# Optimization experiments

Hardware: AMD Instinct MI355X
Metric: run time of the kernel (lower is better)

Reference implementation:

```python
import jax, jax.numpy as jnp
import numpy as np

DT = 1e-3
MAX_UPDATE = 0.1


def setup_inputs() -> dict:
    key = jax.random.key(0)
    k1, k2 = jax.random.split(key)
    B, T = 512, 8192
    inputs = jax.random.normal(k1, (B, T, 2), dtype=jnp.float32)
    # learned 2x2 kernel, keras 'uniform' init ~ U(-0.05, 0.05)
    A = jax.random.uniform(k2, (2, 2), dtype=jnp.float32, minval=-0.05, maxval=0.05)
    # physical model coefficients (from coeffs tuple)
    C = jnp.eye(2, dtype=jnp.float32)
    D = 1e-3 * jnp.eye(2, dtype=jnp.float32)
    return {"inputs": inputs, "A": A, "C": C, "D": D}


def reference(inputs, A, C, D):
    # inputs: [B, T, 2] measurement increments dy
    B = inputs.shape[0]
    # initial state per GRNNmodel.initial_state: x0=[1,0], cov0=eye(2)
    x0 = jnp.tile(jnp.array([[1.0, 0.0]], dtype=inputs.dtype), (B, 1))      # [B,2]
    cov0 = jnp.tile(jnp.eye(2, dtype=inputs.dtype)[None], (B, 1, 1))        # [B,2,2]

    Ct = C.T
    Dt = D.T

    def step(carry, dy):
        x, cov = carry                                   # [B,2], [B,2,2]
        out = jnp.einsum('ij,bj->bi', C, x) * DT         # output uses pre-update state
        xicov = cov @ Ct + Dt                            # [B,2,2]
        A_minus_xiC = A - xicov @ C                      # [B,2,2]
        dx = jnp.einsum('bij,bj->bi', A_minus_xiC, x) * DT \
             + jnp.einsum('bij,bj->bi', xicov, dy)
        x_new = x + jnp.clip(dx, -MAX_UPDATE, MAX_UPDATE)
        cov_dt = (jnp.einsum('ij,bjk->bik', A, cov)
                  + jnp.einsum('bij,kj->bik', cov, A)    # cov @ A^T
                  + D
                  - xicov @ jnp.swapaxes(xicov, 1, 2))
        cov_new = jnp.clip(cov + cov_dt * DT, -1.0, 1.0)
        return (x_new, cov_new), out

    dys = jnp.swapaxes(inputs, 0, 1)                     # [T,B,2]
    _, outs = jax.lax.scan(step, (x0, cov0), dys)
    return jnp.swapaxes(outs, 0, 1)                      # [B,T,2]
```

## Files before the change

kernel.cpp:

```cpp
#include <hip/hip_runtime.h>


#define DT_C 1e-3f
#define MAXU 0.1f
#define T_LEN 8192
#define T4 (T_LEN / 2)
#define CHUNK 256
#define G_CHUNK (CHUNK / 2)
#define NCHUNK (T_LEN / CHUNK)

__device__ __forceinline__ float clipf(float v, float lo, float hi) {
    return fminf(fmaxf(v, lo), hi);
}
#define MEDU(x) __builtin_amdgcn_fmed3f((x), -MAXU, MAXU)
#define SB() __builtin_amdgcn_sched_barrier(0)

__global__ __launch_bounds__(128, 1) void grnn_fused(
    const float* __restrict__ inp, const float* __restrict__ Am,
    const float* __restrict__ Cm, const float* __restrict__ Dm,
    float* __restrict__ out)
{
    __shared__ float pb0[CHUNK + 1];
    __shared__ float pb1[CHUNK + 1];
    __shared__ float pb2[CHUNK + 1];
    __shared__ float4 pbufg[CHUNK];
    __shared__ float4 wlds[2][CHUNK * 2];
    const int tid = threadIdx.x;

    if (tid < 64) {
        const int lane = tid;
        const float a00 = Am[0], a01 = Am[1], a10 = Am[2], a11 = Am[3];
        const float c00 = Cm[0], c01 = Cm[1], c10 = Cm[2], c11 = Cm[3];
        const float d00 = Dm[0], d01 = Dm[1], d10 = Dm[2], d11 = Dm[3];
        const bool special = (c00 == 1.f) && (c01 == 0.f) && (c10 == 0.f) &&
                             (c11 == 1.f) && (d01 == 0.f) && (d10 == 0.f);
        const float adt00 = a00 * DT_C, adt01 = a01 * DT_C;
        const float adt10 = a10 * DT_C, adt11 = a11 * DT_C;

        if (special) {
            const float K00 = 1.f + 2.f * adt00, A2dt01 = 2.f * adt01;
            const float K11 = 1.f + 2.f * adt11, A2dt10 = 2.f * adt10;
            const float K01 = 1.f + (a00 + a11) * DT_C;
            const float cd0 = DT_C * d00, cd1 = DT_C * d11;
            float p00 = 1.f, p01 = 0.f, p11 = 1.f;

#define PSTEP(I)                                                              \
            {                                                                 \
                const float xi00 = p00 + d00;                                 \
                const float xi11 = p11 + d11;                                 \
                const float s2  = p01 * p01;                                  \
                const float q00 = fmaf(xi00, xi00, s2);                       \
                const float q11 = fmaf(xi11, xi11, s2);                       \
                const float q01 = p01 * (xi00 + xi11);                        \
                const float t00 = fmaf(K00, p00, fmaf(A2dt01, p01, cd0));     \
                const float t11 = fmaf(A2dt10, p01, fmaf(K11, p11, cd1));     \
                const float t01 = fmaf(adt10, p00,                            \
                                       fmaf(K01, p01, adt01 * p11));          \
                p00 = fmaf(-DT_C, q00, t00);                                  \
                p01 = fmaf(-DT_C, q01, t01);                                  \
                p11 = fmaf(-DT_C, q11, t11);                                  \
                pb0[(I) + 1] = p00;                                           \
                pb1[(I) + 1] = p01;                                           \
                pb2[(I) + 1] = p11;                                           \
            }

            for (int it = 0; it <= NCHUNK; ++it) {
                if (it < NCHUNK) {
                    if (lane == 0) {
                        pb0[0] = p00; pb1[0] = p01; pb2[0] = p11;
                        for (int i = 0; i < CHUNK; i += 8) {
                            PSTEP(i)     PSTEP(i + 1) PSTEP(i + 2) PSTEP(i + 3)
                            PSTEP(i + 4) PSTEP(i + 5) PSTEP(i + 6) PSTEP(i + 7)
                        }
                    }
                    __builtin_amdgcn_wave_barrier();
                    float4* dst = wlds[it & 1];
#pragma unroll
                    for (int k = 0; k < 4; ++k) {
                        const int i = k * 64 + lane;
                        const float pv0 = pb0[i], pv1 = pb1[i], pv2 = pb2[i];
                        const float xi00 = pv0 + d00, xi01 = pv1, xi11 = pv2 + d11;
                        float4 mv, xv;
                        mv.x = fmaf(-DT_C, xi00, adt00);
                        mv.y = fmaf(-DT_C, xi01, adt10);
                        mv.z = fmaf(-DT_C, xi01, adt01);
                        mv.w = fmaf(-DT_C, xi11, adt11);
                        xv = make_float4(xi00, xi01, xi01, xi11);
                        dst[2 * i]     = mv;
                        dst[2 * i + 1] = xv;
                    }
                }
                __syncthreads();
            }
#undef PSTEP
        } else {
            float p00 = 1.f, p01 = 0.f, p10 = 0.f, p11 = 1.f;
            for (int it = 0; it <= NCHUNK; ++it) {
                if (it < NCHUNK) {
                    if (lane == 0) {
                        for (int i = 0; i < CHUNK; ++i) {
                            pbufg[i] = make_float4(p00, p01, p10, p11);
                            const float xi00 = p00*c00 + p01*c01 + d00;
                            const float xi01 = p00*c10 + p01*c11 + d10;
                            const float xi10 = p10*c00 + p11*c01 + d01;
                            const float xi11 = p10*c10 + p11*c11 + d11;
                            const float g00 = a00*p00 + a01*p10 + p00*a00 + p01*a01 + d00 - (xi00*xi00 + xi01*xi01);
                            const float g01 = a00*p01 + a01*p11 + p00*a10 + p01*a11 + d01 - (xi00*xi10 + xi01*xi11);
                            const float g10 = a10*p00 + a11*p10 + p10*a00 + p11*a01 + d10 - (xi10*xi00 + xi11*xi01);
                            const float g11 = a10*p01 + a11*p11 + p10*a10 + p11*a11 + d11 - (xi10*xi10 + xi11*xi11);
                            p00 = clipf(p00 + g00 * DT_C, -1.f, 1.f);
                            p01 = clipf(p01 + g01 * DT_C, -1.f, 1.f);
                            p10 = clipf(p10 + g10 * DT_C, -1.f, 1.f);
                            p11 = clipf(p11 + g11 * DT_C, -1.f, 1.f);
                        }
                    }
                    __builtin_amdgcn_wave_barrier();
                    float4* dst = wlds[it & 1];
#pragma unroll
                    for (int k = 0; k < 4; ++k) {
                        const int i = k * 64 + lane;
                        const float4 pv = pbufg[i];
                        const float xi00 = pv.x*c00 + pv.y*c01 + d00;
                        const float xi01 = pv.x*c10 + pv.y*c11 + d10;
                        const float xi10 = pv.z*c00 + pv.w*c01 + d01;
                        const float xi11 = pv.z*c10 + pv.w*c11 + d11;
                        const float m00 = a00 - (xi00*c00 + xi01*c10);
                        const float m01 = a01 - (xi00*c01 + xi01*c11);
                        const float m10 = a10 - (xi10*c00 + xi11*c10);
                        const float m11 = a11 - (xi10*c01 + xi11*c11);
                        float4 mv, xv;
                        mv.x = m00 * DT_C; mv.y = m10 * DT_C;
                        mv.z = m01 * DT_C; mv.w = m11 * DT_C;
                        xv = make_float4(xi00, xi10, xi01, xi11);
                        dst[2 * i]     = mv;
                        dst[2 * i + 1] = xv;
                    }
                }
                __syncthreads();
            }
        }
    } else {
        const int lane = tid - 64;
        const int b = blockIdx.x * 64 + lane;
        const float cdt00 = Cm[0] * DT_C, cdt01 = Cm[1] * DT_C;
        const float cdt10 = Cm[2] * DT_C, cdt11 = Cm[3] * DT_C;
        const float4* __restrict__ in4 =
            reinterpret_cast<const float4*>(inp) + (size_t)b * T4;
        float4* __restrict__ out4 =
            reinterpret_cast<float4*>(out) + (size_t)b * T4;

        float x0 = 1.f, x1 = 0.f;
        float4 d0 = in4[0], d1 = in4[1], d2 = in4[2], d3 = in4[3];
        float4 d4 = in4[4], d5 = in4[5], d6 = in4[6], d7 = in4[7];
        float4 s0a, s0b, s0c, s0d, s1a, s1b, s1c, s1d;
        float4 t0a, t0b, t0c, t0d, t1a, t1b, t1c, t1d;

#define WLG(P, G)                                                             \
        { P##a = wbuf[4*(G)];   P##b = wbuf[4*(G)+1];                         \
          P##c = wbuf[4*(G)+2]; P##d = wbuf[4*(G)+3]; }

#define GRANC(P, DJ, OG)                                                      \
        {                                                                     \
            const float4 dyv = DJ;                                            \
            float4 ov;                                                        \
            ov.x = fmaf(cdt00, x0, cdt01 * x1);                               \
            ov.y = fmaf(cdt10, x0, cdt11 * x1);                               \
            float e0 = fmaf(P##b.x, dyv.x, P##b.z * dyv.y);                   \
            float e1 = fmaf(P##b.y, dyv.x, P##b.w * dyv.y);                   \
            float dx0 = fmaf(P##a.x, x0, fmaf(P##a.z, x1, e0));               \
            float dx1 = fmaf(P##a.y, x0, fmaf(P##a.w, x1, e1));               \
            x0 += MEDU(dx0);                                                  \
            x1 += MEDU(dx1);                                                  \
            ov.z = fmaf(cdt00, x0, cdt01 * x1);                               \
            ov.w = fmaf(cdt10, x0, cdt11 * x1);                               \
            e0 = fmaf(P##d.x, dyv.z, P##d.z * dyv.w);                         \
            e1 = fmaf(P##d.y, dyv.z, P##d.w * dyv.w);                         \
            dx0 = fmaf(P##c.x, x0, fmaf(P##c.z, x1, e0));                     \
            dx1 = fmaf(P##c.y, x0, fmaf(P##c.w, x1, e1));                     \
            x0 += MEDU(dx0);                                                  \
            x1 += MEDU(dx1);                                                  \
            out4[OG] = ov;                                                    \
            const int nog = (OG) + 8;                                         \
            DJ = in4[nog < T4 ? nog : (T4 - 1)];                              \
        }

        for (int it = 0; it <= NCHUNK; ++it) {
            if (it > 0) {
                const int cc = it - 1;
                const float4* wbuf = wlds[cc & 1];
                const int ogc = cc * G_CHUNK;
                WLG(s0, 0) WLG(s1, 1)
                SB();
                for (int q = 0; q < G_CHUNK / 8; ++q) {
                    const int g = 8 * q;
                    const int og = ogc + g;
                    WLG(t0, g + 2) WLG(t1, g + 3)
                    SB();
                    GRANC(s0, d0, og)     GRANC(s1, d1, og + 1)
                    SB();
                    WLG(s0, g + 4) WLG(s1, g + 5)
                    SB();
                    GRANC(t0, d2, og + 2) GRANC(t1, d3, og + 3)
                    SB();
                    WLG(t0, g + 6) WLG(t1, g + 7)
                    SB();
                    GRANC(s0, d4, og + 4) GRANC(s1, d5, og + 5)
                    SB();
                    {
                        const int gn0 = (g + 8 < G_CHUNK) ? (g + 8) : (G_CHUNK - 1);
                        const int gn1 = (g + 9 < G_CHUNK) ? (g + 9) : (G_CHUNK - 1);
                        WLG(s0, gn0) WLG(s1, gn1)
                    }
                    SB();
                    GRANC(t0, d6, og + 6) GRANC(t1, d7, og + 7)
                    SB();
                }
            }
            __syncthreads();
        }
#undef GRANC
#undef WLG
    }
}

__global__ __launch_bounds__(64) void grnn_mono(
    const float* __restrict__ inp, const float* __restrict__ Am,
    const float* __restrict__ Cm, const float* __restrict__ Dm,
    float* __restrict__ out, int B)
{
    const int b = blockIdx.x * blockDim.x + threadIdx.x;
    if (b >= B) return;
    const float a00 = Am[0], a01 = Am[1], a10 = Am[2], a11 = Am[3];
    const float c00 = Cm[0], c01 = Cm[1], c10 = Cm[2], c11 = Cm[3];
    const float d00 = Dm[0], d01 = Dm[1], d10 = Dm[2], d11 = Dm[3];
    float x0 = 1.0f, x1 = 0.0f;
    float p00 = 1.0f, p01 = 0.0f, p10 = 0.0f, p11 = 1.0f;
    const float2* __restrict__ in2 = reinterpret_cast<const float2*>(inp) + (size_t)b * T_LEN;
    float2* __restrict__ out2 = reinterpret_cast<float2*>(out) + (size_t)b * T_LEN;
#pragma unroll 4
    for (int t = 0; t < T_LEN; ++t) {
        float2 o;
        o.x = (c00 * x0 + c01 * x1) * DT_C;
        o.y = (c10 * x0 + c11 * x1) * DT_C;
        out2[t] = o;
        const float xi00 = p00 * c00 + p01 * c01 + d00;
        const float xi01 = p00 * c10 + p01 * c11 + d10;
        const float xi10 = p10 * c00 + p11 * c01 + d01;
        const float xi11 = p10 * c10 + p11 * c11 + d11;
        const float m00 = a00 - (xi00 * c00 + xi01 * c10);
        const float m01 = a01 - (xi00 * c01 + xi01 * c11);
        const float m10 = a10 - (xi10 * c00 + xi11 * c10);
        const float m11 = a11 - (xi10 * c01 + xi11 * c11);
        const float2 dy = in2[t];
        float dx0 = (m00 * x0 + m01 * x1) * DT_C + xi00 * dy.x + xi01 * dy.y;
        float dx1 = (m10 * x0 + m11 * x1) * DT_C + xi10 * dy.x + xi11 * dy.y;
        x0 += clipf(dx0, -MAXU, MAXU);
        x1 += clipf(dx1, -MAXU, MAXU);
        const float g00 = a00*p00 + a01*p10 + p00*a00 + p01*a01 + d00 - (xi00*xi00 + xi01*xi01);
        const float g01 = a00*p01 + a01*p11 + p00*a10 + p01*a11 + d01 - (xi00*xi10 + xi01*xi11);
        const float g10 = a10*p00 + a11*p10 + p10*a00 + p11*a01 + d10 - (xi10*xi00 + xi11*xi01);
        const float g11 = a10*p01 + a11*p11 + p10*a10 + p11*a11 + d11 - (xi10*xi10 + xi11*xi11);
        p00 = clipf(p00 + g00 * DT_C, -1.0f, 1.0f);
        p01 = clipf(p01 + g01 * DT_C, -1.0f, 1.0f);
        p10 = clipf(p10 + g10 * DT_C, -1.0f, 1.0f);
        p11 = clipf(p11 + g11 * DT_C, -1.0f, 1.0f);
    }
}

extern "C" void kernel_launch(void* const* d_in, const int* in_sizes, int n_in,
                              void* d_out, int out_size, void* d_ws, size_t ws_size,
                              hipStream_t stream) {
    const float* inp = (const float*)d_in[0];
    const float* Am  = (const float*)d_in[1];
    const float* Cm  = (const float*)d_in[2];
    const float* Dm  = (const float*)d_in[3];
    float* out = (float*)d_out;
    const int B = in_sizes[0] / (T_LEN * 2);

    if ((B % 64) == 0) {
        hipLaunchKernelGGL(grnn_fused, dim3(B / 64), dim3(128), 0, stream,
                           inp, Am, Cm, Dm, out);
    } else {
        hipLaunchKernelGGL(grnn_mono, dim3((B + 63) / 64), dim3(64), 0, stream,
                           inp, Am, Cm, Dm, out, B);
    }
}
```

Baseline: 537.7 us.

## Batch covariance stores into vector LDS writes and add idle waves

The scalar covariance recurrence in lane 0 now collects eight consecutive states in float4 registers and writes them to LDS with vector stores, replacing three scalar stores per step. The shared buffers drop their +1 offset, so each chunk begins with the state before the step. The block grows to four waves: wave 0 runs the per-batch state update, wave 1 produces the covariance, and waves 2 and 3 only join the barriers, which may change how the waves are placed on SIMDs. The next-input global load in the state update is also issued at the start of each step to give it more time in flight.

```diff
diff --git a/kernel.cpp b/kernel.cpp
--- a/kernel.cpp
+++ b/kernel.cpp
@@ -9,26 +9,29 @@
 #define G_CHUNK (CHUNK / 2)
 #define NCHUNK (T_LEN / CHUNK)
 
+typedef float vfloat4 __attribute__((ext_vector_type(4)));
+
 __device__ __forceinline__ float clipf(float v, float lo, float hi) {
     return fminf(fmaxf(v, lo), hi);
 }
 #define MEDU(x) __builtin_amdgcn_fmed3f((x), -MAXU, MAXU)
 #define SB() __builtin_amdgcn_sched_barrier(0)
 
-__global__ __launch_bounds__(128, 1) void grnn_fused(
+__global__ __launch_bounds__(256, 1) void grnn_fused(
     const float* __restrict__ inp, const float* __restrict__ Am,
     const float* __restrict__ Cm, const float* __restrict__ Dm,
     float* __restrict__ out)
 {
-    __shared__ float pb0[CHUNK + 1];
-    __shared__ float pb1[CHUNK + 1];
-    __shared__ float pb2[CHUNK + 1];
+    __shared__ alignas(16) float pb0[CHUNK];
+    __shared__ alignas(16) float pb1[CHUNK];
+    __shared__ alignas(16) float pb2[CHUNK];
     __shared__ float4 pbufg[CHUNK];
     __shared__ float4 wlds[2][CHUNK * 2];
     const int tid = threadIdx.x;
-
-    if (tid < 64) {
-        const int lane = tid;
+    const int wv = tid >> 6;
+
+    if (wv == 1) {
+        const int lane = tid & 63;
         const float a00 = Am[0], a01 = Am[1], a10 = Am[2], a11 = Am[3];
         const float c00 = Cm[0], c01 = Cm[1], c10 = Cm[2], c11 = Cm[3];
         const float d00 = Dm[0], d01 = Dm[1], d10 = Dm[2], d11 = Dm[3];
@@ -44,8 +47,9 @@
             const float cd0 = DT_C * d00, cd1 = DT_C * d11;
             float p00 = 1.f, p01 = 0.f, p11 = 1.f;
 
-#define PSTEP(I)                                                              \
+#define PSTEP(Q0, Q1, Q2, F)                                                  \
             {                                                                 \
+                Q0.F = p00; Q1.F = p01; Q2.F = p11;                           \
                 const float xi00 = p00 + d00;                                 \
                 const float xi11 = p11 + d11;                                 \
                 const float s2  = p01 * p01;                                  \
@@ -59,18 +63,33 @@
                 p00 = fmaf(-DT_C, q00, t00);                                  \
                 p01 = fmaf(-DT_C, q01, t01);                                  \
                 p11 = fmaf(-DT_C, q11, t11);                                  \
-                pb0[(I) + 1] = p00;                                           \
-                pb1[(I) + 1] = p01;                                           \
-                pb2[(I) + 1] = p11;                                           \
+            }
+
+#define PBLOCK8(QA0, QA1, QA2, QB0, QB1, QB2, I)                              \
+            {                                                                 \
+                PSTEP(QA0, QA1, QA2, x) PSTEP(QA0, QA1, QA2, y)               \
+                PSTEP(QA0, QA1, QA2, z) PSTEP(QA0, QA1, QA2, w)               \
+                PSTEP(QB0, QB1, QB2, x) PSTEP(QB0, QB1, QB2, y)               \
+                PSTEP(QB0, QB1, QB2, z) PSTEP(QB0, QB1, QB2, w)               \
+                *(vfloat4*)&pb0[(I)]     = QA0;                               \
+                *(vfloat4*)&pb0[(I) + 4] = QB0;                               \
+                *(vfloat4*)&pb1[(I)]     = QA1;                               \
+                *(vfloat4*)&pb1[(I) + 4] = QB1;                               \
+                *(vfloat4*)&pb2[(I)]     = QA2;                               \
+                *(vfloat4*)&pb2[(I) + 4] = QB2;                               \
             }
 
             for (int it = 0; it <= NCHUNK; ++it) {
                 if (it < NCHUNK) {
                     if (lane == 0) {
-                        pb0[0] = p00; pb1[0] = p01; pb2[0] = p11;
-                        for (int i = 0; i < CHUNK; i += 8) {
-                            PSTEP(i)     PSTEP(i + 1) PSTEP(i + 2) PSTEP(i + 3)
-                            PSTEP(i + 4) PSTEP(i + 5) PSTEP(i + 6) PSTEP(i + 7)
+                        for (int i = 0; i < CHUNK; i += 16) {
+                            vfloat4 qa0, qa1, qa2, qb0, qb1, qb2;
+                            vfloat4 qc0, qc1, qc2, qd0, qd1, qd2;
+                            PBLOCK8(qa0, qa1, qa2, qb0, qb1, qb2, i)
+                            PBLOCK8(qc0, qc1, qc2, qd0, qd1, qd2, i + 8)
+                            asm volatile("" ::
+                                "v"(qa0), "v"(qa1), "v"(qa2),
+                                "v"(qb0), "v"(qb1), "v"(qb2));
                         }
                     }
                     __builtin_amdgcn_wave_barrier();
@@ -92,6 +111,7 @@
                 }
                 __syncthreads();
             }
+#undef PBLOCK8
 #undef PSTEP
         } else {
             float p00 = 1.f, p01 = 0.f, p10 = 0.f, p11 = 1.f;
@@ -139,8 +159,8 @@
                 __syncthreads();
             }
         }
-    } else {
-        const int lane = tid - 64;
+    } else if (wv == 0) {
+        const int lane = tid;
         const int b = blockIdx.x * 64 + lane;
         const float cdt00 = Cm[0] * DT_C, cdt01 = Cm[1] * DT_C;
         const float cdt10 = Cm[2] * DT_C, cdt11 = Cm[3] * DT_C;
@@ -162,6 +182,8 @@
 #define GRANC(P, DJ, OG)                                                      \
         {                                                                     \
             const float4 dyv = DJ;                                            \
+            const int nog = (OG) + 8;                                         \
+            DJ = in4[nog < T4 ? nog : (T4 - 1)];                              \
             float4 ov;                                                        \
             ov.x = fmaf(cdt00, x0, cdt01 * x1);                               \
             ov.y = fmaf(cdt10, x0, cdt11 * x1);                               \
@@ -180,8 +202,6 @@
             x0 += MEDU(dx0);                                                  \
             x1 += MEDU(dx1);                                                  \
             out4[OG] = ov;                                                    \
-            const int nog = (OG) + 8;                                         \
-            DJ = in4[nog < T4 ? nog : (T4 - 1)];                              \
         }
 
         for (int it = 0; it <= NCHUNK; ++it) {
@@ -220,6 +240,8 @@
         }
 #undef GRANC
 #undef WLG
+    } else {
+        for (int it = 0; it <= NCHUNK; ++it) __syncthreads();
     }
 }
 
@@ -278,7 +300,7 @@
     const int B = in_sizes[0] / (T_LEN * 2);
 
     if ((B % 64) == 0) {
-        hipLaunchKernelGGL(grnn_fused, dim3(B / 64), dim3(128), 0, stream,
+        hipLaunchKernelGGL(grnn_fused, dim3(B / 64), dim3(256), 0, stream,
                            inp, Am, Cm, Dm, out);
     } else {
         hipLaunchKernelGGL(grnn_mono, dim3((B + 63) / 64), dim3(64), 0, stream,
```

After: 497.3 us. -7.5%, faster.

## Split fused kernel into covariance precompute, transposed-layout scan, and transpose kernels

Applied to the files above, without the earlier changes.

The fused producer/consumer kernel is replaced by a pipeline of separate kernels. First the batch-independent covariance recurrence runs serially to produce chunk boundary states, while the input is transposed to time-major layout in the same launch. Next, per-step weight tables are expanded in parallel across chunks into global memory. Then a scan kernel reads the transposed inputs with coalesced loads and writes time-major output, and a final kernel transposes the output back. This removes the per-chunk block barriers and LDS handoff and makes the per-step loads coalesced. The cost is extra launches, two full transposes through global memory, and a serial covariance pass that now runs ahead of the scan instead of overlapping with it.

```diff
diff --git a/kernel.cpp b/kernel.cpp
--- a/kernel.cpp
+++ b/kernel.cpp
@@ -6,29 +6,53 @@
 #define T_LEN 8192
 #define T4 (T_LEN / 2)
 #define CHUNK 256
-#define G_CHUNK (CHUNK / 2)
 #define NCHUNK (T_LEN / CHUNK)
+#define BROWS 512
 
 __device__ __forceinline__ float clipf(float v, float lo, float hi) {
     return fminf(fmaxf(v, lo), hi);
 }
 #define MEDU(x) __builtin_amdgcn_fmed3f((x), -MAXU, MAXU)
-#define SB() __builtin_amdgcn_sched_barrier(0)
-
-__global__ __launch_bounds__(128, 1) void grnn_fused(
-    const float* __restrict__ inp, const float* __restrict__ Am,
-    const float* __restrict__ Cm, const float* __restrict__ Dm,
-    float* __restrict__ out)
-{
-    __shared__ float pb0[CHUNK + 1];
-    __shared__ float pb1[CHUNK + 1];
-    __shared__ float pb2[CHUNK + 1];
-    __shared__ float4 pbufg[CHUNK];
-    __shared__ float4 wlds[2][CHUNK * 2];
-    const int tid = threadIdx.x;
-
-    if (tid < 64) {
-        const int lane = tid;
+
+#define RSTEP_S()                                                             \
+    {                                                                         \
+        const float xi00 = p00 + d00;                                         \
+        const float xi11 = p11 + d11;                                         \
+        const float s2   = p01 * p01;                                         \
+        const float q00  = fmaf(xi00, xi00, s2);                              \
+        const float q11  = fmaf(xi11, xi11, s2);                              \
+        const float q01  = p01 * (xi00 + xi11);                               \
+        const float t00  = fmaf(K00, p00, fmaf(A2dt01, p01, cd0));            \
+        const float t11  = fmaf(A2dt10, p01, fmaf(K11, p11, cd1));            \
+        const float t01  = fmaf(adt10, p00, fmaf(K01, p01, adt01 * p11));     \
+        p00 = fmaf(-DT_C, q00, t00);                                          \
+        p01 = fmaf(-DT_C, q01, t01);                                          \
+        p11 = fmaf(-DT_C, q11, t11);                                          \
+    }
+
+#define RSTEP_G()                                                             \
+    {                                                                         \
+        const float xi00 = p00*c00 + p01*c01 + d00;                           \
+        const float xi01 = p00*c10 + p01*c11 + d10;                           \
+        const float xi10 = p10*c00 + p11*c01 + d01;                           \
+        const float xi11 = p10*c10 + p11*c11 + d11;                           \
+        const float g00 = a00*p00 + a01*p10 + p00*a00 + p01*a01 + d00 - (xi00*xi00 + xi01*xi01); \
+        const float g01 = a00*p01 + a01*p11 + p00*a10 + p01*a11 + d01 - (xi00*xi10 + xi01*xi11); \
+        const float g10 = a10*p00 + a11*p10 + p10*a00 + p11*a01 + d10 - (xi10*xi00 + xi11*xi01); \
+        const float g11 = a10*p01 + a11*p11 + p10*a10 + p11*a11 + d11 - (xi10*xi10 + xi11*xi11); \
+        p00 = clipf(p00 + g00 * DT_C, -1.f, 1.f);                             \
+        p01 = clipf(p01 + g01 * DT_C, -1.f, 1.f);                             \
+        p10 = clipf(p10 + g10 * DT_C, -1.f, 1.f);                             \
+        p11 = clipf(p11 + g11 * DT_C, -1.f, 1.f);                             \
+    }
+
+__global__ __launch_bounds__(256) void transpose_in_a1(
+    const float4* __restrict__ src, float4* __restrict__ dst,
+    const float* __restrict__ Am, const float* __restrict__ Cm,
+    const float* __restrict__ Dm, float4* __restrict__ bnd, int do_tr)
+{
+    if ((int)blockIdx.x == (int)gridDim.x - 1) {
+        if (blockIdx.y != 0 || threadIdx.x != 0) return;
         const float a00 = Am[0], a01 = Am[1], a10 = Am[2], a11 = Am[3];
         const float c00 = Cm[0], c01 = Cm[1], c10 = Cm[2], c11 = Cm[3];
         const float d00 = Dm[0], d01 = Dm[1], d10 = Dm[2], d11 = Dm[3];
@@ -36,191 +60,188 @@
                              (c11 == 1.f) && (d01 == 0.f) && (d10 == 0.f);
         const float adt00 = a00 * DT_C, adt01 = a01 * DT_C;
         const float adt10 = a10 * DT_C, adt11 = a11 * DT_C;
-
+        (void)adt00; (void)adt11;
         if (special) {
             const float K00 = 1.f + 2.f * adt00, A2dt01 = 2.f * adt01;
             const float K11 = 1.f + 2.f * adt11, A2dt10 = 2.f * adt10;
             const float K01 = 1.f + (a00 + a11) * DT_C;
             const float cd0 = DT_C * d00, cd1 = DT_C * d11;
             float p00 = 1.f, p01 = 0.f, p11 = 1.f;
-
-#define PSTEP(I)                                                              \
-            {                                                                 \
-                const float xi00 = p00 + d00;                                 \
-                const float xi11 = p11 + d11;                                 \
-                const float s2  = p01 * p01;                                  \
-                const float q00 = fmaf(xi00, xi00, s2);                       \
-                const float q11 = fmaf(xi11, xi11, s2);                       \
-                const float q01 = p01 * (xi00 + xi11);                        \
-                const float t00 = fmaf(K00, p00, fmaf(A2dt01, p01, cd0));     \
-                const float t11 = fmaf(A2dt10, p01, fmaf(K11, p11, cd1));     \
-                const float t01 = fmaf(adt10, p00,                            \
-                                       fmaf(K01, p01, adt01 * p11));          \
-                p00 = fmaf(-DT_C, q00, t00);                                  \
-                p01 = fmaf(-DT_C, q01, t01);                                  \
-                p11 = fmaf(-DT_C, q11, t11);                                  \
-                pb0[(I) + 1] = p00;                                           \
-                pb1[(I) + 1] = p01;                                           \
-                pb2[(I) + 1] = p11;                                           \
+            for (int c = 0; c < NCHUNK; ++c) {
+                bnd[c] = make_float4(p00, p01, p11, 0.f);
+                for (int i = 0; i < CHUNK; i += 8) {
+                    RSTEP_S() RSTEP_S() RSTEP_S() RSTEP_S()
+                    RSTEP_S() RSTEP_S() RSTEP_S() RSTEP_S()
+                }
             }
-
-            for (int it = 0; it <= NCHUNK; ++it) {
-                if (it < NCHUNK) {
-                    if (lane == 0) {
-                        pb0[0] = p00; pb1[0] = p01; pb2[0] = p11;
-                        for (int i = 0; i < CHUNK; i += 8) {
-                            PSTEP(i)     PSTEP(i + 1) PSTEP(i + 2) PSTEP(i + 3)
-                            PSTEP(i + 4) PSTEP(i + 5) PSTEP(i + 6) PSTEP(i + 7)
-                        }
-                    }
-                    __builtin_amdgcn_wave_barrier();
-                    float4* dst = wlds[it & 1];
-#pragma unroll
-                    for (int k = 0; k < 4; ++k) {
-                        const int i = k * 64 + lane;
-                        const float pv0 = pb0[i], pv1 = pb1[i], pv2 = pb2[i];
-                        const float xi00 = pv0 + d00, xi01 = pv1, xi11 = pv2 + d11;
-                        float4 mv, xv;
-                        mv.x = fmaf(-DT_C, xi00, adt00);
-                        mv.y = fmaf(-DT_C, xi01, adt10);
-                        mv.z = fmaf(-DT_C, xi01, adt01);
-                        mv.w = fmaf(-DT_C, xi11, adt11);
-                        xv = make_float4(xi00, xi01, xi01, xi11);
-                        dst[2 * i]     = mv;
-                        dst[2 * i + 1] = xv;
-                    }
-                }
-                __syncthreads();
-            }
-#undef PSTEP
         } else {
             float p00 = 1.f, p01 = 0.f, p10 = 0.f, p11 = 1.f;
-            for (int it = 0; it <= NCHUNK; ++it) {
-                if (it < NCHUNK) {
-                    if (lane == 0) {
-                        for (int i = 0; i < CHUNK; ++i) {
-                            pbufg[i] = make_float4(p00, p01, p10, p11);
-                            const float xi00 = p00*c00 + p01*c01 + d00;
-                            const float xi01 = p00*c10 + p01*c11 + d10;
-                            const float xi10 = p10*c00 + p11*c01 + d01;
-                            const float xi11 = p10*c10 + p11*c11 + d11;
-                            const float g00 = a00*p00 + a01*p10 + p00*a00 + p01*a01 + d00 - (xi00*xi00 + xi01*xi01);
-                            const float g01 = a00*p01 + a01*p11 + p00*a10 + p01*a11 + d01 - (xi00*xi10 + xi01*xi11);
-                            const float g10 = a10*p00 + a11*p10 + p10*a00 + p11*a01 + d10 - (xi10*xi00 + xi11*xi01);
-                            const float g11 = a10*p01 + a11*p11 + p10*a10 + p11*a11 + d11 - (xi10*xi10 + xi11*xi11);
-                            p00 = clipf(p00 + g00 * DT_C, -1.f, 1.f);
-                            p01 = clipf(p01 + g01 * DT_C, -1.f, 1.f);
-                            p10 = clipf(p10 + g10 * DT_C, -1.f, 1.f);
-                            p11 = clipf(p11 + g11 * DT_C, -1.f, 1.f);
-                        }
-                    }
-                    __builtin_amdgcn_wave_barrier();
-                    float4* dst = wlds[it & 1];
-#pragma unroll
-                    for (int k = 0; k < 4; ++k) {
-                        const int i = k * 64 + lane;
-                        const float4 pv = pbufg[i];
-                        const float xi00 = pv.x*c00 + pv.y*c01 + d00;
-                        const float xi01 = pv.x*c10 + pv.y*c11 + d10;
-                        const float xi10 = pv.z*c00 + pv.w*c01 + d01;
-                        const float xi11 = pv.z*c10 + pv.w*c11 + d11;
-                        const float m00 = a00 - (xi00*c00 + xi01*c10);
-                        const float m01 = a01 - (xi00*c01 + xi01*c11);
-                        const float m10 = a10 - (xi10*c00 + xi11*c10);
-                        const float m11 = a11 - (xi10*c01 + xi11*c11);
-                        float4 mv, xv;
-                        mv.x = m00 * DT_C; mv.y = m10 * DT_C;
-                        mv.z = m01 * DT_C; mv.w = m11 * DT_C;
-                        xv = make_float4(xi00, xi10, xi01, xi11);
-                        dst[2 * i]     = mv;
-                        dst[2 * i + 1] = xv;
-                    }
+            for (int c = 0; c < NCHUNK; ++c) {
+                bnd[c] = make_float4(p00, p01, p10, p11);
+                for (int i = 0; i < CHUNK; i += 4) {
+                    RSTEP_G() RSTEP_G() RSTEP_G() RSTEP_G()
                 }
-                __syncthreads();
             }
         }
+        return;
+    }
+    if (!do_tr) return;
+    __shared__ float4 tile[32][33];
+    const int tx = threadIdx.x & 31;
+    const int ty = threadIdx.x >> 5;
+    const int c0 = blockIdx.x * 32;
+    const int r0 = blockIdx.y * 32;
+#pragma unroll
+    for (int i = 0; i < 32; i += 8)
+        tile[ty + i][tx] = src[(size_t)(r0 + ty + i) * T4 + (c0 + tx)];
+    __syncthreads();
+#pragma unroll
+    for (int i = 0; i < 32; i += 8)
+        dst[(size_t)(c0 + ty + i) * BROWS + (r0 + tx)] = tile[tx][ty + i];
+}
+
+__global__ __launch_bounds__(64) void expand_w(
+    const float* __restrict__ Am, const float* __restrict__ Cm,
+    const float* __restrict__ Dm, const float4* __restrict__ bnd,
+    float4* __restrict__ wst)
+{
+    if (threadIdx.x != 0) return;
+    const int c = blockIdx.x;
+    const float a00 = Am[0], a01 = Am[1], a10 = Am[2], a11 = Am[3];
+    const float c00 = Cm[0], c01 = Cm[1], c10 = Cm[2], c11 = Cm[3];
+    const float d00 = Dm[0], d01 = Dm[1], d10 = Dm[2], d11 = Dm[3];
+    const bool special = (c00 == 1.f) && (c01 == 0.f) && (c10 == 0.f) &&
+                         (c11 == 1.f) && (d01 == 0.f) && (d10 == 0.f);
+    const float adt00 = a00 * DT_C, adt01 = a01 * DT_C;
+    const float adt10 = a10 * DT_C, adt11 = a11 * DT_C;
+    float4* wout = wst + (size_t)c * (CHUNK * 2);
+    const float4 s = bnd[c];
+    if (special) {
+        const float K00 = 1.f + 2.f * adt00, A2dt01 = 2.f * adt01;
+        const float K11 = 1.f + 2.f * adt11, A2dt10 = 2.f * adt10;
+        const float K01 = 1.f + (a00 + a11) * DT_C;
+        const float cd0 = DT_C * d00, cd1 = DT_C * d11;
+        float p00 = s.x, p01 = s.y, p11 = s.z;
+#pragma unroll 4
+        for (int i = 0; i < CHUNK; ++i) {
+            const float xi00 = p00 + d00, xi01 = p01, xi11 = p11 + d11;
+            float4 mv, xv;
+            mv.x = fmaf(-DT_C, xi00, adt00);
+            mv.y = fmaf(-DT_C, xi01, adt10);
+            mv.z = fmaf(-DT_C, xi01, adt01);
+            mv.w = fmaf(-DT_C, xi11, adt11);
+            xv = make_float4(xi00, xi01, xi01, xi11);
+            wout[2 * i]     = mv;
+            wout[2 * i + 1] = xv;
+            RSTEP_S()
+        }
     } else {
-        const int lane = tid - 64;
-        const int b = blockIdx.x * 64 + lane;
-        const float cdt00 = Cm[0] * DT_C, cdt01 = Cm[1] * DT_C;
-        const float cdt10 = Cm[2] * DT_C, cdt11 = Cm[3] * DT_C;
-        const float4* __restrict__ in4 =
-            reinterpret_cast<const float4*>(inp) + (size_t)b * T4;
-        float4* __restrict__ out4 =
-            reinterpret_cast<float4*>(out) + (size_t)b * T4;
-
-        float x0 = 1.f, x1 = 0.f;
-        float4 d0 = in4[0], d1 = in4[1], d2 = in4[2], d3 = in4[3];
-        float4 d4 = in4[4], d5 = in4[5], d6 = in4[6], d7 = in4[7];
-        float4 s0a, s0b, s0c, s0d, s1a, s1b, s1c, s1d;
-        float4 t0a, t0b, t0c, t0d, t1a, t1b, t1c, t1d;
-
-#define WLG(P, G)                                                             \
-        { P##a = wbuf[4*(G)];   P##b = wbuf[4*(G)+1];                         \
-          P##c = wbuf[4*(G)+2]; P##d = wbuf[4*(G)+3]; }
+        float p00 = s.x, p01 = s.y, p10 = s.z, p11 = s.w;
+#pragma unroll 4
+        for (int i = 0; i < CHUNK; ++i) {
+            const float xi00 = p00*c00 + p01*c01 + d00;
+            const float xi01 = p00*c10 + p01*c11 + d10;
+            const float xi10 = p10*c00 + p11*c01 + d01;
+            const float xi11 = p10*c10 + p11*c11 + d11;
+            const float m00 = a00 - (xi00*c00 + xi01*c10);
+            const float m01 = a01 - (xi00*c01 + xi01*c11);
+            const float m10 = a10 - (xi10*c00 + xi11*c10);
+            const float m11 = a11 - (xi10*c01 + xi11*c11);
+            float4 mv, xv;
+            mv.x = m00 * DT_C; mv.y = m10 * DT_C;
+            mv.z = m01 * DT_C; mv.w = m11 * DT_C;
+            xv = make_float4(xi00, xi10, xi01, xi11);
+            wout[2 * i]     = mv;
+            wout[2 * i + 1] = xv;
+            RSTEP_G()
+        }
+    }
+}
+
+__global__ __launch_bounds__(64, 1) void grnn_scan(
+    const float4* __restrict__ inA, const float4* __restrict__ wst,
+    const float* __restrict__ Cm, float4* __restrict__ outA, int tr)
+{
+    const int lane = threadIdx.x;
+    const int b = blockIdx.x * 64 + lane;
+    const float cdt00 = Cm[0] * DT_C, cdt01 = Cm[1] * DT_C;
+    const float cdt10 = Cm[2] * DT_C, cdt11 = Cm[3] * DT_C;
+    float x0 = 1.f, x1 = 0.f;
+
+#define IDX(G) (tr ? ((size_t)(G) * BROWS + b) : ((size_t)b * T4 + (G)))
+
+    float4 d0 = inA[IDX(0)], d1 = inA[IDX(1)], d2 = inA[IDX(2)], d3 = inA[IDX(3)];
+    float4 d4 = inA[IDX(4)], d5 = inA[IDX(5)], d6 = inA[IDX(6)], d7 = inA[IDX(7)];
+    float4 s0a, s0b, s0c, s0d, s1a, s1b, s1c, s1d;
+    float4 t0a, t0b, t0c, t0d, t1a, t1b, t1c, t1d;
+    float4 u0a, u0b, u0c, u0d, u1a, u1b, u1c, u1d;
+    float4 v0a, v0b, v0c, v0d, v1a, v1b, v1c, v1d;
+
+#define WLGG(P, G)                                                            \
+    {                                                                         \
+        const int gg = (G) < T4 ? (G) : (T4 - 1);                             \
+        const float4* wp = wst + 4 * (size_t)gg;                              \
+        P##a = wp[0]; P##b = wp[1]; P##c = wp[2]; P##d = wp[3];               \
+    }
 
 #define GRANC(P, DJ, OG)                                                      \
+    {                                                                         \
+        const float4 dyv = DJ;                                                \
         {                                                                     \
-            const float4 dyv = DJ;                                            \
-            float4 ov;                                                        \
-            ov.x = fmaf(cdt00, x0, cdt01 * x1);                               \
-            ov.y = fmaf(cdt10, x0, cdt11 * x1);                               \
-            float e0 = fmaf(P##b.x, dyv.x, P##b.z * dyv.y);                   \
-            float e1 = fmaf(P##b.y, dyv.x, P##b.w * dyv.y);                   \
-            float dx0 = fmaf(P##a.x, x0, fmaf(P##a.z, x1, e0));               \
-            float dx1 = fmaf(P##a.y, x0, fmaf(P##a.w, x1, e1));               \
-            x0 += MEDU(dx0);                                                  \
-            x1 += MEDU(dx1);                                                  \
-            ov.z = fmaf(cdt00, x0, cdt01 * x1);                               \
-            ov.w = fmaf(cdt10, x0, cdt11 * x1);                               \
-            e0 = fmaf(P##d.x, dyv.z, P##d.z * dyv.w);                         \
-            e1 = fmaf(P##d.y, dyv.z, P##d.w * dyv.w);                         \
-            dx0 = fmaf(P##c.x, x0, fmaf(P##c.z, x1, e0));                     \
-            dx1 = fmaf(P##c.y, x0, fmaf(P##c.w, x1, e1));                     \
-            x0 += MEDU(dx0);                                                  \
-            x1 += MEDU(dx1);                                                  \
-            out4[OG] = ov;                                                    \
             const int nog = (OG) + 8;                                         \
-            DJ = in4[nog < T4 ? nog : (T4 - 1)];                              \
-        }
-
-        for (int it = 0; it <= NCHUNK; ++it) {
-            if (it > 0) {
-                const int cc = it - 1;
-                const float4* wbuf = wlds[cc & 1];
-                const int ogc = cc * G_CHUNK;
-                WLG(s0, 0) WLG(s1, 1)
-                SB();
-                for (int q = 0; q < G_CHUNK / 8; ++q) {
-                    const int g = 8 * q;
-                    const int og = ogc + g;
-                    WLG(t0, g + 2) WLG(t1, g + 3)
-                    SB();
-                    GRANC(s0, d0, og)     GRANC(s1, d1, og + 1)
-                    SB();
-                    WLG(s0, g + 4) WLG(s1, g + 5)
-                    SB();
-                    GRANC(t0, d2, og + 2) GRANC(t1, d3, og + 3)
-                    SB();
-                    WLG(t0, g + 6) WLG(t1, g + 7)
-                    SB();
-                    GRANC(s0, d4, og + 4) GRANC(s1, d5, og + 5)
-                    SB();
-                    {
-                        const int gn0 = (g + 8 < G_CHUNK) ? (g + 8) : (G_CHUNK - 1);
-                        const int gn1 = (g + 9 < G_CHUNK) ? (g + 9) : (G_CHUNK - 1);
-                        WLG(s0, gn0) WLG(s1, gn1)
-                    }
-                    SB();
-                    GRANC(t0, d6, og + 6) GRANC(t1, d7, og + 7)
-                    SB();
-                }
-            }
-            __syncthreads();
-        }
+            const int rg = nog < T4 ? nog : (T4 - 1);                         \
+            DJ = inA[IDX(rg)];                                                \
+        }                                                                     \
+        float4 ov;                                                            \
+        ov.x = fmaf(cdt00, x0, cdt01 * x1);                                   \
+        ov.y = fmaf(cdt10, x0, cdt11 * x1);                                   \
+        float e0 = fmaf(P##b.x, dyv.x, P##b.z * dyv.y);                       \
+        float e1 = fmaf(P##b.y, dyv.x, P##b.w * dyv.y);                       \
+        float dx0 = fmaf(P##a.x, x0, fmaf(P##a.z, x1, e0));                   \
+        float dx1 = fmaf(P##a.y, x0, fmaf(P##a.w, x1, e1));                   \
+        x0 += MEDU(dx0);                                                      \
+        x1 += MEDU(dx1);                                                      \
+        ov.z = fmaf(cdt00, x0, cdt01 * x1);                                   \
+        ov.w = fmaf(cdt10, x0, cdt11 * x1);                                   \
+        e0 = fmaf(P##d.x, dyv.z, P##d.z * dyv.w);                             \
+        e1 = fmaf(P##d.y, dyv.z, P##d.w * dyv.w);                             \
+        dx0 = fmaf(P##c.x, x0, fmaf(P##c.z, x1, e0));                         \
+        dx1 = fmaf(P##c.y, x0, fmaf(P##c.w, x1, e1));                         \
+        x0 += MEDU(dx0);                                                      \
+        x1 += MEDU(dx1);                                                      \
+        outA[IDX(OG)] = ov;                                                   \
+    }
+
+    WLGG(s0, 0) WLGG(s1, 1) WLGG(t0, 2) WLGG(t1, 3)
+    WLGG(u0, 4) WLGG(u1, 5) WLGG(v0, 6) WLGG(v1, 7)
+    for (int q = 0; q < T4 / 8; ++q) {
+        const int g = 8 * q;
+        GRANC(s0, d0, g + 0) GRANC(s1, d1, g + 1) WLGG(s0, g + 8)  WLGG(s1, g + 9)
+        GRANC(t0, d2, g + 2) GRANC(t1, d3, g + 3) WLGG(t0, g + 10) WLGG(t1, g + 11)
+        GRANC(u0, d4, g + 4) GRANC(u1, d5, g + 5) WLGG(u0, g + 12) WLGG(u1, g + 13)
+        GRANC(v0, d6, g + 6) GRANC(v1, d7, g + 7) WLGG(v0, g + 14) WLGG(v1, g + 15)
+    }
 #undef GRANC
-#undef WLG
-    }
+#undef WLGG
+#undef IDX
+}
+
+__global__ __launch_bounds__(256) void transpose_f4(
+    const float4* __restrict__ src, float4* __restrict__ dst,
+    int rows, int cols)
+{
+    __shared__ float4 tile[32][33];
+    const int tx = threadIdx.x & 31;
+    const int ty = threadIdx.x >> 5;
+    const int c0 = blockIdx.x * 32;
+    const int r0 = blockIdx.y * 32;
+#pragma unroll
+    for (int i = 0; i < 32; i += 8)
+        tile[ty + i][tx] = src[(size_t)(r0 + ty + i) * cols + (c0 + tx)];
+    __syncthreads();
+#pragma unroll
+    for (int i = 0; i < 32; i += 8)
+        dst[(size_t)(c0 + ty + i) * rows + (r0 + tx)] = tile[tx][ty + i];
 }
 
 __global__ __launch_bounds__(64) void grnn_mono(
@@ -277,9 +298,35 @@
     float* out = (float*)d_out;
     const int B = in_sizes[0] / (T_LEN * 2);
 
-    if ((B % 64) == 0) {
-        hipLaunchKernelGGL(grnn_fused, dim3(B / 64), dim3(128), 0, stream,
-                           inp, Am, Cm, Dm, out);
+    float4* bnd = (float4*)d_ws;
+    float4* wst = bnd + 32;
+    float4* inT  = (float4*)d_ws + 32768;
+    float4* outT = inT + (size_t)T4 * BROWS;
+    const size_t need_mid  = (size_t)(32 + T_LEN * 2) * sizeof(float4);
+    const size_t need_full = (size_t)512 * 1024 +
+                             (size_t)2 * T4 * BROWS * sizeof(float4);
+
+    if (B == BROWS && d_ws != nullptr && ws_size >= need_full) {
+        hipLaunchKernelGGL(transpose_in_a1, dim3(T4 / 32 + 1, BROWS / 32),
+                           dim3(256), 0, stream,
+                           reinterpret_cast<const float4*>(inp), inT,
+                           Am, Cm, Dm, bnd, 1);
+        hipLaunchKernelGGL(expand_w, dim3(NCHUNK), dim3(64), 0, stream,
+                           Am, Cm, Dm, bnd, wst);
+        hipLaunchKernelGGL(grnn_scan, dim3(BROWS / 64), dim3(64), 0, stream,
+                           inT, wst, Cm, outT, 1);
+        hipLaunchKernelGGL(transpose_f4, dim3(BROWS / 32, T4 / 32), dim3(256),
+                           0, stream,
+                           outT, reinterpret_cast<float4*>(out), T4, BROWS);
+    } else if ((B % 64) == 0 && d_ws != nullptr && ws_size >= need_mid) {
+        hipLaunchKernelGGL(transpose_in_a1, dim3(1, 1), dim3(256), 0, stream,
+                           reinterpret_cast<const float4*>(inp), bnd,
+                           Am, Cm, Dm, bnd, 0);
+        hipLaunchKernelGGL(expand_w, dim3(NCHUNK), dim3(64), 0, stream,
+                           Am, Cm, Dm, bnd, wst);
+        hipLaunchKernelGGL(grnn_scan, dim3(B / 64), dim3(64), 0, stream,
+                           reinterpret_cast<const float4*>(inp), wst, Cm,
+                           reinterpret_cast<float4*>(out), 0);
     } else {
         hipLaunchKernelGGL(grnn_mono, dim3((B + 63) / 64), dim3(64), 0, stream,
                            inp, Am, Cm, Dm, out, B);
```

Result: slower. 1.650 ms (+206.8%).

## Transpose inputs/outputs to time-major layout and parallelize covariance chunk expansion

Applied to the files above, without the earlier changes.

Adds a tiled float4 transpose kernel so the recurrence kernel reads and writes time-major data, making per-step global accesses across the 64 batch lanes coalesced instead of strided by the whole sequence length. The covariance producer now runs a serial scan that only records a state every 8 steps, and 32 lanes then recompute the 8 intermediate steps in parallel to fill the shared buffer. The recurrence is also rewritten in terms of xi (u, v, w) with precomputed constants. The trade-off is two extra transpose passes over 32 MB each way plus workspace use, and the fast path is limited to B equal to 512.

```diff
diff --git a/kernel.cpp b/kernel.cpp
--- a/kernel.cpp
+++ b/kernel.cpp
@@ -8,6 +8,7 @@
 #define CHUNK 256
 #define G_CHUNK (CHUNK / 2)
 #define NCHUNK (T_LEN / CHUNK)
+#define BROWS 512
 
 __device__ __forceinline__ float clipf(float v, float lo, float hi) {
     return fminf(fmaxf(v, lo), hi);
@@ -15,20 +16,36 @@
 #define MEDU(x) __builtin_amdgcn_fmed3f((x), -MAXU, MAXU)
 #define SB() __builtin_amdgcn_sched_barrier(0)
 
-__global__ __launch_bounds__(128, 1) void grnn_fused(
-    const float* __restrict__ inp, const float* __restrict__ Am,
+__global__ __launch_bounds__(256) void transpose_f4(
+    const float4* __restrict__ src, float4* __restrict__ dst,
+    int rows, int cols)
+{
+    __shared__ float4 tile[32][33];
+    const int tx = threadIdx.x & 31;
+    const int ty = threadIdx.x >> 5;
+    const int c0 = blockIdx.x * 32;
+    const int r0 = blockIdx.y * 32;
+#pragma unroll
+    for (int i = 0; i < 32; i += 8)
+        tile[ty + i][tx] = src[(size_t)(r0 + ty + i) * cols + (c0 + tx)];
+    __syncthreads();
+#pragma unroll
+    for (int i = 0; i < 32; i += 8)
+        dst[(size_t)(c0 + ty + i) * rows + (r0 + tx)] = tile[tx][ty + i];
+}
+
+__global__ __launch_bounds__(128, 1) void grnn_fused2(
+    const float4* __restrict__ inT, const float* __restrict__ Am,
     const float* __restrict__ Cm, const float* __restrict__ Dm,
-    float* __restrict__ out)
+    float4* __restrict__ outT)
 {
-    __shared__ float pb0[CHUNK + 1];
-    __shared__ float pb1[CHUNK + 1];
-    __shared__ float pb2[CHUNK + 1];
-    __shared__ float4 pbufg[CHUNK];
     __shared__ float4 wlds[2][CHUNK * 2];
+    __shared__ float4 sbnd[CHUNK / 8];
     const int tid = threadIdx.x;
-
-    if (tid < 64) {
-        const int lane = tid;
+    const int wv = tid >> 6;
+
+    if (wv == 1) {
+        const int lane = tid & 63;
         const float a00 = Am[0], a01 = Am[1], a10 = Am[2], a11 = Am[3];
         const float c00 = Cm[0], c01 = Cm[1], c10 = Cm[2], c11 = Cm[3];
         const float d00 = Dm[0], d01 = Dm[1], d10 = Dm[2], d11 = Dm[3];
@@ -41,127 +58,150 @@
             const float K00 = 1.f + 2.f * adt00, A2dt01 = 2.f * adt01;
             const float K11 = 1.f + 2.f * adt11, A2dt10 = 2.f * adt10;
             const float K01 = 1.f + (a00 + a11) * DT_C;
-            const float cd0 = DT_C * d00, cd1 = DT_C * d11;
-            float p00 = 1.f, p01 = 0.f, p11 = 1.f;
-
-#define PSTEP(I)                                                              \
+            const float C0u = DT_C * d00 * (1.f - 2.f * a00);
+            const float C0v = DT_C * d11 * (1.f - 2.f * a11);
+            const float C1w = -(adt10 * d00 + adt01 * d11);
+
+#define XSTEP()                                                               \
             {                                                                 \
-                const float xi00 = p00 + d00;                                 \
-                const float xi11 = p11 + d11;                                 \
-                const float s2  = p01 * p01;                                  \
-                const float q00 = fmaf(xi00, xi00, s2);                       \
-                const float q11 = fmaf(xi11, xi11, s2);                       \
-                const float q01 = p01 * (xi00 + xi11);                        \
-                const float t00 = fmaf(K00, p00, fmaf(A2dt01, p01, cd0));     \
-                const float t11 = fmaf(A2dt10, p01, fmaf(K11, p11, cd1));     \
-                const float t01 = fmaf(adt10, p00,                            \
-                                       fmaf(K01, p01, adt01 * p11));          \
-                p00 = fmaf(-DT_C, q00, t00);                                  \
-                p01 = fmaf(-DT_C, q01, t01);                                  \
-                p11 = fmaf(-DT_C, q11, t11);                                  \
-                pb0[(I) + 1] = p00;                                           \
-                pb1[(I) + 1] = p01;                                           \
-                pb2[(I) + 1] = p11;                                           \
-            }
-
+                const float w2 = w * w;                                       \
+                const float gu = fmaf(-DT_C, u, K00);                         \
+                const float gv = fmaf(-DT_C, v, K11);                         \
+                const float s  = u + v;                                       \
+                const float ru = fmaf(A2dt01, w, fmaf(-DT_C, w2, C0u));       \
+                const float rv = fmaf(A2dt10, w, fmaf(-DT_C, w2, C0v));       \
+                const float gw = fmaf(-DT_C, s, K01);                         \
+                const float rw = fmaf(adt10, u, fmaf(adt01, v, C1w));         \
+                const float un = fmaf(u, gu, ru);                             \
+                const float vn = fmaf(v, gv, rv);                             \
+                const float wn = fmaf(w, gw, rw);                             \
+                u = un; v = vn; w = wn;                                       \
+            }
+
+            float u = 1.f + d00, w = 0.f, v = 1.f + d11;
             for (int it = 0; it <= NCHUNK; ++it) {
                 if (it < NCHUNK) {
                     if (lane == 0) {
-                        pb0[0] = p00; pb1[0] = p01; pb2[0] = p11;
-                        for (int i = 0; i < CHUNK; i += 8) {
-                            PSTEP(i)     PSTEP(i + 1) PSTEP(i + 2) PSTEP(i + 3)
-                            PSTEP(i + 4) PSTEP(i + 5) PSTEP(i + 6) PSTEP(i + 7)
+                        for (int j = 0; j < CHUNK / 8; ++j) {
+                            sbnd[j] = make_float4(u, w, v, 0.f);
+                            XSTEP() XSTEP() XSTEP() XSTEP()
+                            XSTEP() XSTEP() XSTEP() XSTEP()
                         }
                     }
+                    asm volatile("s_waitcnt lgkmcnt(0)" ::: "memory");
+                    SB();
                     __builtin_amdgcn_wave_barrier();
-                    float4* dst = wlds[it & 1];
+                    if (lane < CHUNK / 8) {
+                        const float4 sb = sbnd[lane];
+                        float u2 = sb.x, w2v = sb.y, v2 = sb.z;
+                        float4* wdst = wlds[it & 1] + 2 * (lane * 8);
 #pragma unroll
-                    for (int k = 0; k < 4; ++k) {
-                        const int i = k * 64 + lane;
-                        const float pv0 = pb0[i], pv1 = pb1[i], pv2 = pb2[i];
-                        const float xi00 = pv0 + d00, xi01 = pv1, xi11 = pv2 + d11;
-                        float4 mv, xv;
-                        mv.x = fmaf(-DT_C, xi00, adt00);
-                        mv.y = fmaf(-DT_C, xi01, adt10);
-                        mv.z = fmaf(-DT_C, xi01, adt01);
-                        mv.w = fmaf(-DT_C, xi11, adt11);
-                        xv = make_float4(xi00, xi01, xi01, xi11);
-                        dst[2 * i]     = mv;
-                        dst[2 * i + 1] = xv;
+                        for (int k = 0; k < 8; ++k) {
+                            float4 mv, xv;
+                            mv.x = fmaf(-DT_C, u2, adt00);
+                            mv.y = fmaf(-DT_C, w2v, adt10);
+                            mv.z = fmaf(-DT_C, w2v, adt01);
+                            mv.w = fmaf(-DT_C, v2, adt11);
+                            xv = make_float4(u2, w2v, w2v, v2);
+                            wdst[2 * k]     = mv;
+                            wdst[2 * k + 1] = xv;
+                            {
+                                float u = u2, w = w2v, v = v2;
+                                XSTEP()
+                                u2 = u; w2v = w; v2 = v;
+                            }
+                        }
                     }
                 }
                 __syncthreads();
             }
-#undef PSTEP
+#undef XSTEP
         } else {
+#define RSTEP_G()                                                             \
+            {                                                                 \
+                const float xi00 = p00*c00 + p01*c01 + d00;                   \
+                const float xi01 = p00*c10 + p01*c11 + d10;                   \
+                const float xi10 = p10*c00 + p11*c01 + d01;                   \
+                const float xi11 = p10*c10 + p11*c11 + d11;                   \
+                const float g00 = a00*p00 + a01*p10 + p00*a00 + p01*a01 + d00 - (xi00*xi00 + xi01*xi01); \
+                const float g01 = a00*p01 + a01*p11 + p00*a10 + p01*a11 + d01 - (xi00*xi10 + xi01*xi11); \
+                const float g10 = a10*p00 + a11*p10 + p10*a00 + p11*a01 + d10 - (xi10*xi00 + xi11*xi01); \
+                const float g11 = a10*p01 + a11*p11 + p10*a10 + p11*a11 + d11 - (xi10*xi10 + xi11*xi11); \
+                p00 = clipf(p00 + g00 * DT_C, -1.f, 1.f);                     \
+                p01 = clipf(p01 + g01 * DT_C, -1.f, 1.f);                     \
+                p10 = clipf(p10 + g10 * DT_C, -1.f, 1.f);                     \
+                p11 = clipf(p11 + g11 * DT_C, -1.f, 1.f);                     \
+            }
             float p00 = 1.f, p01 = 0.f, p10 = 0.f, p11 = 1.f;
             for (int it = 0; it <= NCHUNK; ++it) {
                 if (it < NCHUNK) {
                     if (lane == 0) {
-                        for (int i = 0; i < CHUNK; ++i) {
-                            pbufg[i] = make_float4(p00, p01, p10, p11);
+                        for (int j = 0; j < CHUNK / 8; ++j) {
+                            sbnd[j] = make_float4(p00, p01, p10, p11);
+                            RSTEP_G() RSTEP_G() RSTEP_G() RSTEP_G()
+                            RSTEP_G() RSTEP_G() RSTEP_G() RSTEP_G()
+                        }
+                    }
+                    asm volatile("s_waitcnt lgkmcnt(0)" ::: "memory");
+                    SB();
+                    __builtin_amdgcn_wave_barrier();
+                    if (lane < CHUNK / 8) {
+                        const float4 sb = sbnd[lane];
+                        float p00 = sb.x, p01 = sb.y, p10 = sb.z, p11 = sb.w;
+                        float4* wdst = wlds[it & 1] + 2 * (lane * 8);
+#pragma unroll
+                        for (int k = 0; k < 8; ++k) {
                             const float xi00 = p00*c00 + p01*c01 + d00;
                             const float xi01 = p00*c10 + p01*c11 + d10;
                             const float xi10 = p10*c00 + p11*c01 + d01;
                             const float xi11 = p10*c10 + p11*c11 + d11;
-                            const float g00 = a00*p00 + a01*p10 + p00*a00 + p01*a01 + d00 - (xi00*xi00 + xi01*xi01);
-                            const float g01 = a00*p01 + a01*p11 + p00*a10 + p01*a11 + d01 - (xi00*xi10 + xi01*xi11);
-                            const float g10 = a10*p00 + a11*p10 + p10*a00 + p11*a01 + d10 - (xi10*xi00 + xi11*xi01);
-                            const float g11 = a10*p01 + a11*p11 + p10*a10 + p11*a11 + d11 - (xi10*xi10 + xi11*xi11);
-                            p00 = clipf(p00 + g00 * DT_C, -1.f, 1.f);
-                            p01 = clipf(p01 + g01 * DT_C, -1.f, 1.f);
-                            p10 = clipf(p10 + g10 * DT_C, -1.f, 1.f);
-                            p11 = clipf(p11 + g11 * DT_C, -1.f, 1.f);
+                            const float m00 = a00 - (xi00*c00 + xi01*c10);
+                            const float m01 = a01 - (xi00*c01 + xi01*c11);
+                            const float m10 = a10 - (xi10*c00 + xi11*c10);
+                            const float m11 = a11 - (xi10*c01 + xi11*c11);
+                            float4 mv, xv;
+                            mv.x = m00 * DT_C; mv.y = m10 * DT_C;
+                            mv.z = m01 * DT_C; mv.w = m11 * DT_C;
+                            xv = make_float4(xi00, xi10, xi01, xi11);
+                            wdst[2 * k]     = mv;
+                            wdst[2 * k + 1] = xv;
+                            RSTEP_G()
                         }
-                    }
-                    __builtin_amdgcn_wave_barrier();
-                    float4* dst = wlds[it & 1];
-#pragma unroll
-                    for (int k = 0; k < 4; ++k) {
-                        const int i = k * 64 + lane;
-                        const float4 pv = pbufg[i];
-                        const float xi00 = pv.x*c00 + pv.y*c01 + d00;
-                        const float xi01 = pv.x*c10 + pv.y*c11 + d10;
-                        const float xi10 = pv.z*c00 + pv.w*c01 + d01;
-                        const float xi11 = pv.z*c10 + pv.w*c11 + d11;
-                        const float m00 = a00 - (xi00*c00 + xi01*c10);
-                        const float m01 = a01 - (xi00*c01 + xi01*c11);
-                        const float m10 = a10 - (xi10*c00 + xi11*c10);
-                        const float m11 = a11 - (xi10*c01 + xi11*c11);
-                        float4 mv, xv;
-                        mv.x = m00 * DT_C; mv.y = m10 * DT_C;
-                        mv.z = m01 * DT_C; mv.w = m11 * DT_C;
-                        xv = make_float4(xi00, xi10, xi01, xi11);
-                        dst[2 * i]     = mv;
-                        dst[2 * i + 1] = xv;
                     }
                 }
                 __syncthreads();
             }
+#undef RSTEP_G
         }
     } else {
-        const int lane = tid - 64;
+        const int lane = tid;
         const int b = blockIdx.x * 64 + lane;
         const float cdt00 = Cm[0] * DT_C, cdt01 = Cm[1] * DT_C;
         const float cdt10 = Cm[2] * DT_C, cdt11 = Cm[3] * DT_C;
-        const float4* __restrict__ in4 =
-            reinterpret_cast<const float4*>(inp) + (size_t)b * T4;
-        float4* __restrict__ out4 =
-            reinterpret_cast<float4*>(out) + (size_t)b * T4;
-
         float x0 = 1.f, x1 = 0.f;
-        float4 d0 = in4[0], d1 = in4[1], d2 = in4[2], d3 = in4[3];
-        float4 d4 = in4[4], d5 = in4[5], d6 = in4[6], d7 = in4[7];
+
+#define IDX(G) ((size_t)(G) * BROWS + b)
+
+        float4 d0 = inT[IDX(0)], d1 = inT[IDX(1)], d2 = inT[IDX(2)], d3 = inT[IDX(3)];
+        float4 d4 = inT[IDX(4)], d5 = inT[IDX(5)], d6 = inT[IDX(6)], d7 = inT[IDX(7)];
         float4 s0a, s0b, s0c, s0d, s1a, s1b, s1c, s1d;
         float4 t0a, t0b, t0c, t0d, t1a, t1b, t1c, t1d;
 
 #define WLG(P, G)                                                             \
-        { P##a = wbuf[4*(G)];   P##b = wbuf[4*(G)+1];                         \
-          P##c = wbuf[4*(G)+2]; P##d = wbuf[4*(G)+3]; }
+        {                                                                     \
+            const int gg = (G) < G_CHUNK ? (G) : (G_CHUNK - 1);               \
+            const float4* wp = wbuf + 4 * gg;                                 \
+            P##a = wp[0]; P##b = wp[1]; P##c = wp[2]; P##d = wp[3];           \
+        }
 
 #define GRANC(P, DJ, OG)                                                      \
         {                                                                     \
             const float4 dyv = DJ;                                            \
+            {                                                                 \
+                const int nog = (OG) + 8;                                     \
+                const int rg = nog < T4 ? nog : (T4 - 1);                     \
+                DJ = inT[IDX(rg)];                                            \
+            }                                                                 \
             float4 ov;                                                        \
             ov.x = fmaf(cdt00, x0, cdt01 * x1);                               \
             ov.y = fmaf(cdt10, x0, cdt11 * x1);                               \
@@ -179,9 +219,7 @@
             dx1 = fmaf(P##c.y, x0, fmaf(P##c.w, x1, e1));                     \
             x0 += MEDU(dx0);                                                  \
             x1 += MEDU(dx1);                                                  \
-            out4[OG] = ov;                                                    \
-            const int nog = (OG) + 8;                                         \
-            DJ = in4[nog < T4 ? nog : (T4 - 1)];                              \
+            outT[IDX(OG)] = ov;                                               \
         }
 
         for (int it = 0; it <= NCHUNK; ++it) {
@@ -189,37 +227,26 @@
                 const int cc = it - 1;
                 const float4* wbuf = wlds[cc & 1];
                 const int ogc = cc * G_CHUNK;
-                WLG(s0, 0) WLG(s1, 1)
+                WLG(s0, 0) WLG(s1, 1) WLG(t0, 2) WLG(t1, 3)
                 SB();
                 for (int q = 0; q < G_CHUNK / 8; ++q) {
                     const int g = 8 * q;
                     const int og = ogc + g;
-                    WLG(t0, g + 2) WLG(t1, g + 3)
-                    SB();
-                    GRANC(s0, d0, og)     GRANC(s1, d1, og + 1)
-                    SB();
-                    WLG(s0, g + 4) WLG(s1, g + 5)
-                    SB();
-                    GRANC(t0, d2, og + 2) GRANC(t1, d3, og + 3)
-                    SB();
-                    WLG(t0, g + 6) WLG(t1, g + 7)
-                    SB();
-                    GRANC(s0, d4, og + 4) GRANC(s1, d5, og + 5)
-                    SB();
-                    {
-                        const int gn0 = (g + 8 < G_CHUNK) ? (g + 8) : (G_CHUNK - 1);
-                        const int gn1 = (g + 9 < G_CHUNK) ? (g + 9) : (G_CHUNK - 1);
-                        WLG(s0, gn0) WLG(s1, gn1)
-                    }
-                    SB();
-                    GRANC(t0, d6, og + 6) GRANC(t1, d7, og + 7)
-                    SB();
+                    GRANC(s0, d0, og + 0) GRANC(s1, d1, og + 1) SB();
+                    WLG(s0, g + 4) WLG(s1, g + 5) SB();
+                    GRANC(t0, d2, og + 2) GRANC(t1, d3, og + 3) SB();
+                    WLG(t0, g + 6) WLG(t1, g + 7) SB();
+                    GRANC(s0, d4, og + 4) GRANC(s1, d5, og + 5) SB();
+                    WLG(s0, g + 8) WLG(s1, g + 9) SB();
+                    GRANC(t0, d6, og + 6) GRANC(t1, d7, og + 7) SB();
+                    WLG(t0, g + 10) WLG(t1, g + 11) SB();
                 }
             }
             __syncthreads();
         }
 #undef GRANC
 #undef WLG
+#undef IDX
     }
 }
 
@@ -277,9 +304,20 @@
     float* out = (float*)d_out;
     const int B = in_sizes[0] / (T_LEN * 2);
 
-    if ((B % 64) == 0) {
-        hipLaunchKernelGGL(grnn_fused, dim3(B / 64), dim3(128), 0, stream,
-                           inp, Am, Cm, Dm, out);
+    float4* inT  = (float4*)d_ws;
+    float4* outT = inT + (size_t)T4 * BROWS;
+    const size_t need_ws = (size_t)2 * T4 * BROWS * sizeof(float4);
+
+    if (B == BROWS && d_ws != nullptr && ws_size >= need_ws) {
+        hipLaunchKernelGGL(transpose_f4, dim3(T4 / 32, BROWS / 32), dim3(256),
+                           0, stream,
+                           reinterpret_cast<const float4*>(inp), inT,
+                           BROWS, T4);
+        hipLaunchKernelGGL(grnn_fused2, dim3(BROWS / 64), dim3(128), 0,
+                           stream, inT, Am, Cm, Dm, outT);
+        hipLaunchKernelGGL(transpose_f4, dim3(BROWS / 32, T4 / 32), dim3(256),
+                           0, stream,
+                           outT, reinterpret_cast<float4*>(out), T4, BROWS);
     } else {
         hipLaunchKernelGGL(grnn_mono, dim3((B + 63) / 64), dim3(64), 0, stream,
                            inp, Am, Cm, Dm, out, B);
```

Result: faster. 514.0 us (-4.4%).
